# Performance work log

Hardware: AMD Instinct MI355X
Metric: run time of the kernel (lower is better)

Reference implementation:

```python
import jax, jax.numpy as jnp
import numpy as np

B, S, D = 2, 1024, 4096
N_HEADS, KV_HEADS, HEAD_DIM = 32, 8, 128
EPS = 1e-6
ROPE_THETA = 1e6


def setup_inputs() -> dict:
    key = jax.random.key(0)
    ks = jax.random.split(key, 7)
    scale = 0.02
    x = jax.random.normal(ks[0], (B, S, D), dtype=jnp.float32)
    positions = jnp.broadcast_to(jnp.arange(S, dtype=jnp.int32)[None, :], (B, S))
    wq = jax.random.normal(ks[1], (D, N_HEADS, HEAD_DIM), dtype=jnp.float32) * scale
    wk = jax.random.normal(ks[2], (D, KV_HEADS, HEAD_DIM), dtype=jnp.float32) * scale
    wv = jax.random.normal(ks[3], (D, KV_HEADS, HEAD_DIM), dtype=jnp.float32) * scale
    wo = jax.random.normal(ks[4], (N_HEADS, HEAD_DIM, D), dtype=jnp.float32) * scale
    q_norm_w = 1.0 + jax.random.normal(ks[5], (HEAD_DIM,), dtype=jnp.float32) * 0.01
    k_norm_w = 1.0 + jax.random.normal(ks[6], (HEAD_DIM,), dtype=jnp.float32) * 0.01
    return {"x": x, "positions": positions, "wq": wq, "wk": wk, "wv": wv,
            "wo": wo, "q_norm_w": q_norm_w, "k_norm_w": k_norm_w}


def _rms_norm(t, w):
    # per-head RMSNorm over last (head_dim) axis
    var = jnp.mean(jnp.square(t), axis=-1, keepdims=True)
    return (t * jax.lax.rsqrt(var + EPS)) * w


def _rope(t, positions):
    # neox-style rotary embedding; t: [B, S, n, H], positions: [B, S]
    half = t.shape[-1] // 2
    inv_freq = 1.0 / (ROPE_THETA ** (jnp.arange(0, half, dtype=jnp.float32) / half))
    ang = positions.astype(jnp.float32)[..., None] * inv_freq  # [B, S, half]
    cos = jnp.cos(ang)[:, :, None, :]  # [B, S, 1, half]
    sin = jnp.sin(ang)[:, :, None, :]
    t1, t2 = t[..., :half], t[..., half:]
    return jnp.concatenate([t1 * cos - t2 * sin, t2 * cos + t1 * sin], axis=-1)


def reference(x, positions, wq, wk, wv, wo, q_norm_w, k_norm_w):
    # QKV projections (einsum layers: 'bsd,dnh->bsnh')
    q = jnp.einsum('bsd,dnh->bsnh', x, wq)  # [B, S, N, H]
    k = jnp.einsum('bsd,dkh->bskh', x, wk)  # [B, S, K, H]
    v = jnp.einsum('bsd,dkh->bskh', x, wv)
    # per-head QK RMSNorm, then RoPE
    q = _rope(_rms_norm(q, q_norm_w), positions)
    k = _rope(_rms_norm(k, k_norm_w), positions)
    # GQA: expand KV heads to query heads
    groups = N_HEADS // KV_HEADS
    k = jnp.repeat(k, groups, axis=2)  # [B, S, N, H]
    v = jnp.repeat(v, groups, axis=2)
    sm_scale = HEAD_DIM ** -0.5
    scores = jnp.einsum('bqnh,btnh->bnqt', q, k) * sm_scale  # [B, N, S, S]
    causal = jnp.tril(jnp.ones((S, S), dtype=bool))
    scores = jnp.where(causal[None, None], scores, jnp.finfo(scores.dtype).min)
    probs = jax.nn.softmax(scores, axis=-1)
    attn = jnp.einsum('bnqt,btnh->bqnh', probs, v)  # [B, S, N, H]
    out = jnp.einsum('bqnh,nhd->bqd', attn, wo)  # output projection
    return out
```

## Files before the change

kernel.cpp:

```cpp
#include <hip/hip_runtime.h>
#include <stdint.h>

#define S_LEN   1024
#define D_MODEL 4096
#define NHQ     32
#define NKV     8
#define HD      128
#define NTOK    2048
#define NQKV    6144
#define SM_SCALE 0.08838834764831843f
#define LOG2E    1.4426950408889634f

typedef __attribute__((ext_vector_type(8))) __bf16 bf16x8;
typedef __attribute__((ext_vector_type(4))) float f32x4;

__device__ __forceinline__ unsigned short f2bf(float f) {
  union { float f; unsigned u; } x; x.f = f;
  unsigned r = x.u + 0x7fffu + ((x.u >> 16) & 1u);
  return (unsigned short)(r >> 16);
}
__device__ __forceinline__ float bf2f(unsigned short u) {
  union { unsigned u; float f; } x; x.u = (unsigned)u << 16; return x.f;
}

__device__ __forceinline__ void gload_lds16(const void* g, void* l) {
  __builtin_amdgcn_global_load_lds((__attribute__((address_space(1))) void*)g,
                                   (__attribute__((address_space(3))) void*)l,
                                   16, 0, 0);
}

__global__ void k_f32_to_bf16(const float* __restrict__ in,
                              unsigned short* __restrict__ out, int n8) {
  int i = blockIdx.x * blockDim.x + threadIdx.x;
  if (i >= n8) return;
  const float4* p = (const float4*)(in + (size_t)i * 8);
  float4 v0 = p[0], v1 = p[1];
  uint4 o;
  o.x = f2bf(v0.x) | ((unsigned)f2bf(v0.y) << 16);
  o.y = f2bf(v0.z) | ((unsigned)f2bf(v0.w) << 16);
  o.z = f2bf(v1.x) | ((unsigned)f2bf(v1.y) << 16);
  o.w = f2bf(v1.z) | ((unsigned)f2bf(v1.w) << 16);
  *(uint4*)(out + (size_t)i * 8) = o;
}

__global__ void k_transpose(const float* __restrict__ in,
                            unsigned short* __restrict__ out, int R, int C) {
  __shared__ float t[32][33];
  int c = threadIdx.x & 31, r0 = threadIdx.x >> 5;
  int cb = blockIdx.x * 32, rb = blockIdx.y * 32;
#pragma unroll
  for (int i = 0; i < 4; ++i) {
    int r = r0 + i * 8;
    t[r][c] = in[(size_t)(rb + r) * C + cb + c];
  }
  __syncthreads();
#pragma unroll
  for (int i = 0; i < 4; ++i) {
    int r = r0 + i * 8;
    out[(size_t)(cb + r) * R + rb + c] = f2bf(t[c][r]);
  }
}


#define LGKM0 { asm volatile("s_waitcnt lgkmcnt(0)" ::: "memory"); \
                __builtin_amdgcn_sched_barrier(0); }
#define SCHED __builtin_amdgcn_sched_barrier(0);
#define BAR   __builtin_amdgcn_s_barrier();
#define GATE  { if constexpr (NF == 4)                                          \
                  asm volatile("s_waitcnt vmcnt(4)" ::: "memory");              \
                else                                                            \
                  asm volatile("s_waitcnt vmcnt(3)" ::: "memory"); }

#define STGA(h, bufb, kOff)                                                     \
  _Pragma("unroll")                                                             \
  for (int i_ = 0; i_ < 2; ++i_)                                                \
    gload_lds16(gA[i_] + (kOff) + (h) * 64,                                     \
                smem + (bufb) + (h) * 16384 + dA[i_]);

#define STGB(h, bufb, kOff)                                                     \
  _Pragma("unroll")                                                             \
  for (int i_ = 0; i_ < NF / 2; ++i_)                                           \
    gload_lds16(gB[i_] + (kOff) + (h) * 64,                                     \
                smem + (bufb) + 32768 + (h) * (NF * 4096) + dB[i_]);

#define RD_A(dst, mh, kh, bufb)                                                 \
  _Pragma("unroll")                                                             \
  for (int mf = 0; mf < 4; ++mf) {                                              \
    int row = wr * 128 + (mh) * 64 + mf * 16 + lr;                              \
    dst[mf] = *(const bf16x8*)(smem + (bufb) + (kh) * 16384 + row * 64          \
                               + ((lg * 16) ^ (((row >> 1) & 3) << 4)));        \
  }

#define RD_B(dst, kh, bufb)                                                     \
  _Pragma("unroll")                                                             \
  for (int nf = 0; nf < NF; ++nf) {                                             \
    int row = wc * (NF * 16) + nf * 16 + lr;                                    \
    dst[nf] = *(const bf16x8*)(smem + (bufb) + 32768 + (kh) * (NF * 4096)       \
                               + row * 64 + ((lg * 16) ^ (((row >> 1) & 3) << 4))); \
  }

#define MFMA16(mh, AF, BF)                                                      \
  __builtin_amdgcn_s_setprio(1);                                                \
  _Pragma("unroll")                                                             \
  for (int mf = 0; mf < 4; ++mf)                                                \
    _Pragma("unroll")                                                           \
    for (int nf = 0; nf < NF; ++nf)                                             \
      acc[(mh) * 4 + mf][nf] = __builtin_amdgcn_mfma_f32_16x16x32_bf16(         \
          AF[mf], BF[nf], acc[(mh) * 4 + mf][nf], 0, 0, 0);                     \
  __builtin_amdgcn_s_setprio(0);

template <int NF, typename OutT>
__global__ __launch_bounds__(512, 1) void k_gemm256(
    const unsigned short* __restrict__ Aptr,
    const unsigned short* __restrict__ Bptr,
    OutT* __restrict__ C,
    int Kstride, int ldc, int NT, int SGN, int nxn) {
  extern __shared__ __align__(16) char smem[];
  constexpr int BUFST = 32768 + NF * 8192;
  int tid = threadIdx.x;
  int l = tid & 63;
  int w = tid >> 6;
  int lr = l & 15, lg = l >> 4;
  int wr = w >> 2, wc = w & 3;
  int per_xcd = gridDim.x >> 3;
  int x8 = blockIdx.x & 7, i = blockIdx.x >> 3;
  int SGM = per_xcd / SGN;
  int xr = x8 / nxn, xc = x8 - xr * nxn;
  int iy = i / SGN;
  int by = xr * SGM + iy, bx = xc * SGN + (i - iy * SGN);
  int bm = by * 256, bn = bx * (NF * 64);

  const char* gA[2]; int dA[2];
#pragma unroll
  for (int i_ = 0; i_ < 2; ++i_) {
    int lin = i_ * 512 + tid;
    int r_ = lin >> 2, slot = lin & 3, sw = slot ^ ((r_ >> 1) & 3);
    gA[i_] = (const char*)(Aptr + (size_t)(bm + r_) * Kstride) + sw * 16;
    dA[i_] = lin * 16;
  }
  const char* gB[NF / 2]; int dB[NF / 2];
#pragma unroll
  for (int i_ = 0; i_ < NF / 2; ++i_) {
    int lin = i_ * 512 + tid;
    int r_ = lin >> 2, slot = lin & 3, sw = slot ^ ((r_ >> 1) & 3);
    gB[i_] = (const char*)(Bptr + (size_t)(bn + r_) * Kstride) + sw * 16;
    dB[i_] = lin * 16;
  }

  f32x4 acc[8][NF] = {};
  bf16x8 afA[4], afB[4], bfA[NF], bfB[NF];

  STGA(0, 0, 0) STGB(0, 0, 0)
  STGA(1, 0, 0) STGB(1, 0, 0)
  GATE
  BAR
  RD_A(afA, 0, 0, 0) RD_B(bfA, 0, 0)

  for (int kt = 0; kt < NT; ++kt) {
    int curb = (kt & 1) * BUFST;
    int nxtb = BUFST - curb;
    int kOff = (kt + 1) * 128;
    STGA(0, nxtb, kOff)
    BAR LGKM0
    RD_A(afB, 1, 0, curb) SCHED
    MFMA16(0, afA, bfA)
    BAR
    STGB(0, nxtb, kOff)
    GATE BAR LGKM0
    RD_A(afA, 0, 1, curb) RD_B(bfB, 1, curb) SCHED
    MFMA16(1, afB, bfA)
    BAR
    STGA(1, nxtb, kOff)
    BAR LGKM0
    RD_A(afB, 1, 1, curb) SCHED
    MFMA16(0, afA, bfB)
    BAR
    STGB(1, nxtb, kOff)
    GATE BAR LGKM0
    RD_A(afA, 0, 0, nxtb) RD_B(bfA, 0, nxtb) SCHED
    MFMA16(1, afB, bfB)
    BAR
  }

#pragma unroll
  for (int mh = 0; mh < 2; ++mh)
#pragma unroll
    for (int mf = 0; mf < 4; ++mf)
#pragma unroll
      for (int nf = 0; nf < NF; ++nf)
#pragma unroll
        for (int j = 0; j < 4; ++j) {
          size_t idx = (size_t)(bm + wr * 128 + mh * 64 + mf * 16 + lg * 4 + j) * ldc +
                       bn + wc * (NF * 16) + nf * 16 + lr;
          float v = acc[mh * 4 + mf][nf][j];
          if constexpr (sizeof(OutT) == 2) C[idx] = f2bf(v);
          else C[idx] = v;
        }
}

__global__ void k_norm_rope(const unsigned short* __restrict__ qkv,
                            const float* __restrict__ w,
                            const int* __restrict__ positions,
                            unsigned short* __restrict__ out, int nheads, int colbase,
                            float oscale) {
  int wid = blockIdx.x * 4 + (threadIdx.x >> 6);
  int lane = threadIdx.x & 63;
  int token = wid / nheads, head = wid - token * nheads;
  const unsigned short* src = qkv + (size_t)token * NQKV + colbase + head * HD;
  float e0 = bf2f(src[lane]), e1 = bf2f(src[lane + 64]);
  float ss = e0 * e0 + e1 * e1;
#pragma unroll
  for (int m = 1; m < 64; m <<= 1) ss += __shfl_xor(ss, m, 64);
  float rs = rsqrtf(ss * (1.0f / 128.0f) + 1e-6f);
  float n0 = e0 * rs * w[lane], n1 = e1 * rs * w[lane + 64];
  int pos = positions[token];
  float invf = exp2f((float)lane * (-19.931568569324174f / 64.0f));
  float ang = (float)pos * invf;
  float sv, cv;
  sincosf(ang, &sv, &cv);
  float o0 = (n0 * cv - n1 * sv) * oscale;
  float o1 = (n1 * cv + n0 * sv) * oscale;
  int b = token >> 10, s = token & 1023;
  size_t ob = ((size_t)(b * nheads + head) * S_LEN + s) * HD;
  out[ob + lane] = f2bf(o0);
  out[ob + 64 + lane] = f2bf(o1);
}

__global__ void k_v_transpose(const unsigned short* __restrict__ qkv,
                              unsigned short* __restrict__ vt) {
  __shared__ unsigned short t[32][33];
  int slice = blockIdx.z;
  int b = slice >> 3, kh = slice & 7;
  const unsigned short* in = qkv + (size_t)(b * S_LEN) * NQKV + 5120 + kh * HD;
  unsigned short* out = vt + (size_t)slice * HD * S_LEN;
  int c = threadIdx.x & 31, r0 = threadIdx.x >> 5;
  int s0 = blockIdx.y * 32, d0 = blockIdx.x * 32;
#pragma unroll
  for (int i = 0; i < 4; ++i) {
    int r = r0 + i * 8;
    t[r][c] = in[(size_t)(s0 + r) * NQKV + d0 + c];
  }
  __syncthreads();
#pragma unroll
  for (int i = 0; i < 4; ++i) {
    int r = r0 + i * 8;
    out[(size_t)(d0 + r) * S_LEN + s0 + c] = t[c][r];
  }
}

__global__ __launch_bounds__(512) void k_attn(const unsigned short* __restrict__ qh,
                                              const unsigned short* __restrict__ kbuf,
                                              const unsigned short* __restrict__ vtbuf,
                                              unsigned short* __restrict__ attn_out) {
  __shared__ __align__(16) unsigned short k_lds[64 * 128];
  __shared__ __align__(16) unsigned short v_lds[128 * 64];
  __shared__ __align__(16) unsigned short p_lds[8][16 * 64];
  int b = blockIdx.z, h = blockIdx.y, bx = blockIdx.x;
  int khd = h >> 2;
  int tid = threadIdx.x, w = tid >> 6, l = tid & 63;
  int lr = l & 15, lg = l >> 4;
  const unsigned short* K = kbuf + (size_t)(b * NKV + khd) * S_LEN * HD;
  const unsigned short* VT = vtbuf + (size_t)(b * NKV + khd) * HD * S_LEN;
  char* klp = (char*)k_lds;
  char* vlp = (char*)v_lds;
  char* plp = (char*)p_lds[w];
  int swz = (lr & 7) << 4;

  for (int strip = 0; strip < 2; ++strip) {
    int qs = strip ? (7 - bx) : bx;
    int q0 = qs * 128;
    int rbase = q0 + w * 16;
    const unsigned short* Q = qh + ((size_t)(b * NHQ + h) * S_LEN + rbase) * HD;
    bf16x8 qf[4];
#pragma unroll
    for (int kk = 0; kk < 4; ++kk)
      qf[kk] = *(const bf16x8*)&Q[(size_t)lr * HD + kk * 32 + lg * 8];

    f32x4 o[8] = {};
    float m_[4], l_[4];
#pragma unroll
    for (int j = 0; j < 4; ++j) { m_[j] = -1e30f; l_[j] = 0.0f; }

    int nt = 2 * qs + 2;
    for (int t = 0; t < nt; ++t) {
      int t0 = t * 64;
      __syncthreads();
#pragma unroll
      for (int it = 0; it < 2; ++it) {
        int db = (tid + it * 512) * 16;
        int kr = db >> 8, kc = db & 255;
        gload_lds16(K + (size_t)(t0 + kr) * HD + ((kc ^ ((kr & 7) << 4)) >> 1), klp + db);
        int vr = db >> 7, vc = db & 127;
        gload_lds16(VT + (size_t)vr * S_LEN + t0 + ((vc ^ ((vr & 7) << 4)) >> 1), vlp + db);
      }
      __syncthreads();

      f32x4 sc[4];
      __builtin_amdgcn_s_setprio(1);
#pragma unroll
      for (int ct = 0; ct < 4; ++ct) {
        f32x4 s = {};
        int row = ct * 16 + lr;
#pragma unroll
        for (int kk = 0; kk < 4; ++kk) {
          bf16x8 kf = *(const bf16x8*)(klp + row * 256 + ((kk * 64 + lg * 16) ^ swz));
          s = __builtin_amdgcn_mfma_f32_16x16x32_bf16(qf[kk], kf, s, 0, 0, 0);
        }
        sc[ct] = s;
      }
      __builtin_amdgcn_s_setprio(0);

      bool fullw = (t0 + 63 <= rbase);
      float alpha[4];
#pragma unroll
      for (int j = 0; j < 4; ++j) {
        if (!fullw) {
          int rg = rbase + lg * 4 + j;
#pragma unroll
          for (int ct = 0; ct < 4; ++ct)
            sc[ct][j] = (t0 + ct * 16 + lr <= rg) ? sc[ct][j] : -1e30f;
        }
        float mx = fmaxf(fmaxf(sc[0][j], sc[1][j]), fmaxf(sc[2][j], sc[3][j]));
#pragma unroll
        for (int msk = 1; msk < 16; msk <<= 1) mx = fmaxf(mx, __shfl_xor(mx, msk, 64));
        float mn = fmaxf(m_[j], mx);
        alpha[j] = exp2f(m_[j] - mn);
        int q = lg * 4 + j;
        int psw = (q & 7) << 4;
        float ps = 0.0f;
#pragma unroll
        for (int ct = 0; ct < 4; ++ct) {
          float p = exp2f(sc[ct][j] - mn);
          ps += p;
          *(unsigned short*)(plp + q * 128 + (((ct * 16 + lr) * 2) ^ psw)) = f2bf(p);
        }
#pragma unroll
        for (int msk = 1; msk < 16; msk <<= 1) ps += __shfl_xor(ps, msk, 64);
        l_[j] = l_[j] * alpha[j] + ps;
        m_[j] = mn;
      }
#pragma unroll
      for (int dc = 0; dc < 8; ++dc) {
        o[dc][0] *= alpha[0]; o[dc][1] *= alpha[1];
        o[dc][2] *= alpha[2]; o[dc][3] *= alpha[3];
      }
      asm volatile("s_waitcnt lgkmcnt(0)" ::: "memory");
      __builtin_amdgcn_s_setprio(1);
#pragma unroll
      for (int kt = 0; kt < 2; ++kt) {
        bf16x8 pa = *(const bf16x8*)(plp + lr * 128 + ((kt * 64 + lg * 16) ^ swz));
#pragma unroll
        for (int dc = 0; dc < 8; ++dc) {
          int vrow = dc * 16 + lr;
          bf16x8 vf = *(const bf16x8*)(vlp + vrow * 128 + ((kt * 64 + lg * 16) ^ swz));
          o[dc] = __builtin_amdgcn_mfma_f32_16x16x32_bf16(pa, vf, o[dc], 0, 0, 0);
        }
      }
      __builtin_amdgcn_s_setprio(0);
    }

#pragma unroll
    for (int j = 0; j < 4; ++j) {
      int rg = rbase + lg * 4 + j;
      size_t row = (size_t)(b * S_LEN + rg) * D_MODEL + h * HD;
      float inv = 1.0f / l_[j];
#pragma unroll
      for (int dc = 0; dc < 8; ++dc)
        attn_out[row + dc * 16 + lr] = f2bf(o[dc][j] * inv);
    }
  }
}

extern "C" void kernel_launch(void* const* d_in, const int* in_sizes, int n_in,
                              void* d_out, int out_size, void* d_ws, size_t ws_size,
                              hipStream_t stream) {
  const float* x        = (const float*)d_in[0];
  const int* positions  = (const int*)d_in[1];
  const float* wq       = (const float*)d_in[2];
  const float* wk       = (const float*)d_in[3];
  const float* wv       = (const float*)d_in[4];
  const float* wo       = (const float*)d_in[5];
  const float* qnw      = (const float*)d_in[6];
  const float* knw      = (const float*)d_in[7];
  float* out            = (float*)d_out;

  char* ws = (char*)d_ws;
  unsigned short* xb   = (unsigned short*)(ws);
  unsigned short* wB   = (unsigned short*)(ws + 16777216);
  unsigned short* woT  = (unsigned short*)(ws + 67108864);
  unsigned short* qkvb = (unsigned short*)(ws + 100663296);
  unsigned short* qh   = wB;
  unsigned short* khb  = (unsigned short*)(ws + 33554432);
  unsigned short* vtb  = (unsigned short*)(ws + 37748736);
  unsigned short* attn = xb;

  dim3 tb(256);
  k_f32_to_bf16<<<4096, tb, 0, stream>>>(x, xb, 1048576);
  k_transpose<<<dim3(128, 128), tb, 0, stream>>>(wq, wB, 4096, 4096);
  k_transpose<<<dim3(32, 128), tb, 0, stream>>>(wk, wB + (size_t)4096 * 4096, 4096, 1024);
  k_transpose<<<dim3(32, 128), tb, 0, stream>>>(wv, wB + (size_t)5120 * 4096, 4096, 1024);
  k_transpose<<<dim3(128, 128), tb, 0, stream>>>(wo, woT, 4096, 4096);

  k_gemm256<4, unsigned short><<<dim3(192), dim3(512), 131072, stream>>>(
      xb, wB, qkvb, 4096, 6144, 64, 6, 4);

  k_norm_rope<<<16384, tb, 0, stream>>>(qkvb, qnw, positions, qh, 32, 0, SM_SCALE * LOG2E);
  k_norm_rope<<<4096, tb, 0, stream>>>(qkvb, knw, positions, khb, 8, 4096, 1.0f);
  k_v_transpose<<<dim3(4, 32, 16), tb, 0, stream>>>(qkvb, vtb);

  k_attn<<<dim3(4, 32, 2), dim3(512), 0, stream>>>(qh, khb, vtb, attn);

  k_gemm256<2, float><<<dim3(256), dim3(512), 98304, stream>>>(
      attn, woT, out, 4096, 4096, 64, 8, 4);
}
```

Before: 331.8 us.

## Restructure GEMM main loop into a flat two-stage prefetch-ahead pipeline

The GEMM main loop is rewritten so that global-to-LDS loads run two k-tiles ahead into the buffer being consumed, instead of ping-ponging between a current and a next buffer. Each half-k step now reads all eight A fragments and the B fragments at once, then issues a full 8xNF MFMA block, replacing the interleaved 4-fragment half-steps. The vmcnt gates are widened to allow more loads in flight. This cuts the number of barriers and the fine-grained interleaving, at the cost of more live fragment registers and a clamped redundant reload on the final iterations.

```diff
diff --git a/kernel.cpp b/kernel.cpp
--- a/kernel.cpp
+++ b/kernel.cpp
@@ -64,12 +64,11 @@
 
 #define LGKM0 { asm volatile("s_waitcnt lgkmcnt(0)" ::: "memory"); \
                 __builtin_amdgcn_sched_barrier(0); }
-#define SCHED __builtin_amdgcn_sched_barrier(0);
 #define BAR   __builtin_amdgcn_s_barrier();
 #define GATE  { if constexpr (NF == 4)                                          \
-                  asm volatile("s_waitcnt vmcnt(4)" ::: "memory");              \
+                  asm volatile("s_waitcnt vmcnt(8)" ::: "memory");              \
                 else                                                            \
-                  asm volatile("s_waitcnt vmcnt(3)" ::: "memory"); }
+                  asm volatile("s_waitcnt vmcnt(6)" ::: "memory"); }
 
 #define STGA(h, bufb, kOff)                                                     \
   _Pragma("unroll")                                                             \
@@ -83,12 +82,12 @@
     gload_lds16(gB[i_] + (kOff) + (h) * 64,                                     \
                 smem + (bufb) + 32768 + (h) * (NF * 4096) + dB[i_]);
 
-#define RD_A(dst, mh, kh, bufb)                                                 \
+#define RD_A8(dst, kh, bufb)                                                    \
   _Pragma("unroll")                                                             \
-  for (int mf = 0; mf < 4; ++mf) {                                              \
-    int row = wr * 128 + (mh) * 64 + mf * 16 + lr;                              \
-    dst[mf] = *(const bf16x8*)(smem + (bufb) + (kh) * 16384 + row * 64          \
-                               + ((lg * 16) ^ (((row >> 1) & 3) << 4)));        \
+  for (int f = 0; f < 8; ++f) {                                                 \
+    int row = wr * 128 + f * 16 + lr;                                           \
+    dst[f] = *(const bf16x8*)(smem + (bufb) + (kh) * 16384 + row * 64           \
+                              + ((lg * 16) ^ (((row >> 1) & 3) << 4)));         \
   }
 
 #define RD_B(dst, kh, bufb)                                                     \
@@ -99,18 +98,18 @@
                                + row * 64 + ((lg * 16) ^ (((row >> 1) & 3) << 4))); \
   }
 
-#define MFMA16(mh, AF, BF)                                                      \
+#define MFMA32(AF, BF)                                                          \
   __builtin_amdgcn_s_setprio(1);                                                \
   _Pragma("unroll")                                                             \
-  for (int mf = 0; mf < 4; ++mf)                                                \
+  for (int f = 0; f < 8; ++f)                                                   \
     _Pragma("unroll")                                                           \
     for (int nf = 0; nf < NF; ++nf)                                             \
-      acc[(mh) * 4 + mf][nf] = __builtin_amdgcn_mfma_f32_16x16x32_bf16(         \
-          AF[mf], BF[nf], acc[(mh) * 4 + mf][nf], 0, 0, 0);                     \
+      acc[f][nf] = __builtin_amdgcn_mfma_f32_16x16x32_bf16(                     \
+          AF[f], BF[nf], acc[f][nf], 0, 0, 0);                                  \
   __builtin_amdgcn_s_setprio(0);
 
 template <int NF, typename OutT>
-__global__ __launch_bounds__(512, 1) void k_gemm256(
+__global__ __launch_bounds__(512, 1) void k_gemmfl(
     const unsigned short* __restrict__ Aptr,
     const unsigned short* __restrict__ Bptr,
     OutT* __restrict__ C,
@@ -148,54 +147,43 @@
   }
 
   f32x4 acc[8][NF] = {};
-  bf16x8 afA[4], afB[4], bfA[NF], bfB[NF];
+  bf16x8 af[8], bf[NF];
 
   STGA(0, 0, 0) STGB(0, 0, 0)
   STGA(1, 0, 0) STGB(1, 0, 0)
-  GATE
-  BAR
-  RD_A(afA, 0, 0, 0) RD_B(bfA, 0, 0)
+  STGA(0, BUFST, 128) STGB(0, BUFST, 128)
+  STGA(1, BUFST, 128) STGB(1, BUFST, 128)
 
   for (int kt = 0; kt < NT; ++kt) {
     int curb = (kt & 1) * BUFST;
-    int nxtb = BUFST - curb;
-    int kOff = (kt + 1) * 128;
-    STGA(0, nxtb, kOff)
-    BAR LGKM0
-    RD_A(afB, 1, 0, curb) SCHED
-    MFMA16(0, afA, bfA)
+    int kcl = (kt + 2 < NT) ? kt + 2 : NT - 1;
+    int kOff = kcl * 128;
+    GATE
     BAR
-    STGB(0, nxtb, kOff)
-    GATE BAR LGKM0
-    RD_A(afA, 0, 1, curb) RD_B(bfB, 1, curb) SCHED
-    MFMA16(1, afB, bfA)
+    RD_A8(af, 0, curb) RD_B(bf, 0, curb)
+    LGKM0
     BAR
-    STGA(1, nxtb, kOff)
-    BAR LGKM0
-    RD_A(afB, 1, 1, curb) SCHED
-    MFMA16(0, afA, bfB)
+    STGA(0, curb, kOff) STGB(0, curb, kOff)
+    MFMA32(af, bf)
+    RD_A8(af, 1, curb) RD_B(bf, 1, curb)
+    LGKM0
     BAR
-    STGB(1, nxtb, kOff)
-    GATE BAR LGKM0
-    RD_A(afA, 0, 0, nxtb) RD_B(bfA, 0, nxtb) SCHED
-    MFMA16(1, afB, bfB)
-    BAR
-  }
-
-#pragma unroll
-  for (int mh = 0; mh < 2; ++mh)
-#pragma unroll
-    for (int mf = 0; mf < 4; ++mf)
-#pragma unroll
-      for (int nf = 0; nf < NF; ++nf)
-#pragma unroll
-        for (int j = 0; j < 4; ++j) {
-          size_t idx = (size_t)(bm + wr * 128 + mh * 64 + mf * 16 + lg * 4 + j) * ldc +
-                       bn + wc * (NF * 16) + nf * 16 + lr;
-          float v = acc[mh * 4 + mf][nf][j];
-          if constexpr (sizeof(OutT) == 2) C[idx] = f2bf(v);
-          else C[idx] = v;
-        }
+    STGA(1, curb, kOff) STGB(1, curb, kOff)
+    MFMA32(af, bf)
+  }
+
+#pragma unroll
+  for (int f = 0; f < 8; ++f)
+#pragma unroll
+    for (int nf = 0; nf < NF; ++nf)
+#pragma unroll
+      for (int j = 0; j < 4; ++j) {
+        size_t idx = (size_t)(bm + wr * 128 + f * 16 + lg * 4 + j) * ldc +
+                     bn + wc * (NF * 16) + nf * 16 + lr;
+        float v = acc[f][nf][j];
+        if constexpr (sizeof(OutT) == 2) C[idx] = f2bf(v);
+        else C[idx] = v;
+      }
 }
 
 __global__ void k_norm_rope(const unsigned short* __restrict__ qkv,
@@ -401,7 +389,7 @@
   k_transpose<<<dim3(32, 128), tb, 0, stream>>>(wv, wB + (size_t)5120 * 4096, 4096, 1024);
   k_transpose<<<dim3(128, 128), tb, 0, stream>>>(wo, woT, 4096, 4096);
 
-  k_gemm256<4, unsigned short><<<dim3(192), dim3(512), 131072, stream>>>(
+  k_gemmfl<4, unsigned short><<<dim3(192), dim3(512), 131072, stream>>>(
       xb, wB, qkvb, 4096, 6144, 64, 6, 4);
 
   k_norm_rope<<<16384, tb, 0, stream>>>(qkvb, qnw, positions, qh, 32, 0, SM_SCALE * LOG2E);
@@ -410,6 +398,6 @@
 
   k_attn<<<dim3(4, 32, 2), dim3(512), 0, stream>>>(qh, khb, vtb, attn);
 
-  k_gemm256<2, float><<<dim3(256), dim3(512), 98304, stream>>>(
+  k_gemmfl<2, float><<<dim3(256), dim3(512), 98304, stream>>>(
       attn, woT, out, 4096, 4096, 64, 8, 4);
 }
```

Result: no change. 329.1 us (-0.8%).
